# Kernel optimization log

Hardware: AMD Instinct MI355X
Metric: run time of the kernel (lower is better)

Reference implementation:

```python
import jax, jax.numpy as jnp
import numpy as np


def setup_inputs() -> dict:
    key = jax.random.key(0)
    ks = jax.random.split(key, 16)
    B, T, E, H, V = 64, 24, 512, 1024, 32000
    A = H  # attention_dim == hidden_size in original init
    s = 0.02  # init scale
    n = lambda k, shape: (jax.random.normal(k, shape, jnp.float32) * s)
    return {
        "features": jax.random.normal(ks[0], (B, E), jnp.float32),
        "captions": jax.random.randint(ks[1], (B, T), 0, V, dtype=jnp.int32),
        "lengths": jnp.full((B, 1), T + 1, dtype=jnp.int32),
        # learned parameters
        "emb": n(ks[2], (V, E)),
        "We": n(ks[3], (E, A)), "be": jnp.zeros((A,), jnp.float32),
        "Wd": n(ks[4], (H, A)), "bd": jnp.zeros((A,), jnp.float32),
        "va": n(ks[5], (A,)), "ba": jnp.zeros((), jnp.float32),
        "Wih": n(ks[6], (E, H)), "bih": jnp.zeros((H,), jnp.float32),
        "Wic": n(ks[7], (E, H)), "bic": jnp.zeros((H,), jnp.float32),
        "Wfb": n(ks[8], (H, E)), "bfb": jnp.zeros((E,), jnp.float32),
        "Wi": n(ks[9], (2 * E, 4 * H)), "Wh": n(ks[10], (H, 4 * H)),
        "bl": jnp.zeros((4 * H,), jnp.float32),
        "Wo": n(ks[11], (H, V)), "bo": jnp.zeros((V,), jnp.float32),
    }


def reference(features, captions, lengths, emb, We, be, Wd, bd, va, ba,
              Wih, bih, Wic, bic, Wfb, bfb, Wi, Wh, bl, Wo, bo):
    T = captions.shape[1]
    # embeddings = [features ; embed(captions)] -> [B, T+1, E]
    embeds = jnp.concatenate([features[:, None, :], emb[captions]], axis=1)
    mean_e = embeds.mean(axis=1)
    h = mean_e @ Wih + bih  # init_h
    c = mean_e @ Wic + bic  # init_c
    att1 = embeds @ We + be  # encoder projection, precomputed [B, L, A]

    def step(carry, emb_t):
        h, c = carry
        # additive attention over the full encoded sequence
        score = jnp.einsum('bla,a->bl', jax.nn.relu(att1 + (h @ Wd + bd)[:, None, :]), va) + ba
        alpha = jax.nn.softmax(score, axis=1)
        awe = jnp.einsum('bl,ble->be', alpha, embeds)
        gate = jax.nn.sigmoid(h @ Wfb + bfb)
        x = jnp.concatenate([emb_t, gate * awe], axis=-1)  # [B, 2E]
        z = x @ Wi + h @ Wh + bl
        i, f, g, o = jnp.split(z, 4, axis=-1)  # torch LSTM gate order i,f,g,o
        c = jax.nn.sigmoid(f) * c + jax.nn.sigmoid(i) * jnp.tanh(g)
        h = jax.nn.sigmoid(o) * jnp.tanh(c)
        return (h, c), h @ Wo + bo

    emb_seq = jnp.swapaxes(embeds[:, :T, :], 0, 1)  # [T, B, E]
    (_, _), logits = jax.lax.scan(step, (h, c), emb_seq)
    return jnp.swapaxes(logits, 0, 1)  # [B, T, V]
```

## Files before the change

### kernel.cpp

```cpp
#include <hip/hip_runtime.h>
#include <cstdio>
#include <cstdint>

#define B_ 64
#define T_ 24
#define L_ 25
#define E_ 512
#define H_ 1024
#define A_ 1024
#define V_ 32000
#define HCAT 5632

#define NKY_H 12
#define NKY_Z 6

typedef unsigned short u16;
typedef short bf16x8 __attribute__((ext_vector_type(8)));
typedef float f32x4 __attribute__((ext_vector_type(4)));

__device__ __forceinline__ u16 f2bf(float f) {
    union { float f; unsigned int u; } v; v.f = f;
    unsigned int u = v.u;
    unsigned int r = (u + 0x7FFFu + ((u >> 16) & 1u)) >> 16;
    return (u16)r;
}
__device__ __forceinline__ float bf2f(u16 h) {
    union { unsigned int u; float f; } v; v.u = ((unsigned int)h) << 16;
    return v.f;
}
__device__ __forceinline__ void splitbf(float a, u16& hi, u16& lo) {
    hi = f2bf(a);
    lo = f2bf(a - bf2f(hi));
}
__device__ __forceinline__ float sigf(float x) { return 1.f / (1.f + __expf(-x)); }

__device__ __forceinline__ void gload16(const u16* g, u16* l) {
    __builtin_amdgcn_global_load_lds(
        (const __attribute__((address_space(1))) unsigned int*)g,
        (__attribute__((address_space(3))) unsigned int*)l, 16, 0, 0);
}


__global__ void build_embeds(const float* __restrict__ features, const int* __restrict__ captions,
                             const float* __restrict__ emb, float* __restrict__ embeds,
                             float* __restrict__ mean_eT, u16* __restrict__ embsL2,
                             u16* __restrict__ embsA2) {
    int b = blockIdx.x; int e = threadIdx.x;
    float s = 0.f;
    for (int l = 0; l < L_; ++l) {
        float w;
        if (l == 0) w = features[b * E_ + e];
        else {
            int cap = captions[b * T_ + (l - 1)];
            w = emb[(size_t)cap * E_ + e];
        }
        embeds[(size_t)(b * L_ + l) * E_ + e] = w;
        s += w;
        u16 hi, lo; splitbf(w, hi, lo);
        size_t rl = (size_t)(b * L_ + l) * 1536;
        embsL2[rl + e] = hi; embsL2[rl + 512 + e] = lo; embsL2[rl + 1024 + e] = hi;
        if (l < T_) {
            size_t ra = (size_t)(l * 64 + b) * 1536;
            embsA2[ra + e] = hi; embsA2[ra + 512 + e] = lo; embsA2[ra + 1024 + e] = hi;
        }
    }
    mean_eT[e * B_ + b] = s * (1.f / 25.f);
}

__global__ __launch_bounds__(256) void prep_weights(
    const float* __restrict__ Wo, const float* __restrict__ Wd, const float* __restrict__ Wfb,
    const float* __restrict__ Wh, const float* __restrict__ Wi, const float* __restrict__ We,
    u16* __restrict__ WoT, u16* __restrict__ WcatT2, u16* __restrict__ WiT2a,
    u16* __restrict__ WiT2b, u16* __restrict__ WeT2) {
    __shared__ float tile[32][33];
    int id = blockIdx.x;
    int tid = threadIdx.x, tx = tid & 31, ty = tid >> 5;
    if (id < 32000) {
        int nx = id % 1000, ky = id / 1000;
        int n0 = nx * 32, k0 = ky * 32;
        for (int i = ty; i < 32; i += 8)
            tile[i][tx] = Wo[(size_t)(k0 + i) * V_ + n0 + tx];
        __syncthreads();
        for (int i = ty; i < 32; i += 8)
            WoT[(size_t)(n0 + i) * H_ + k0 + tx] = f2bf(tile[tx][i]);
        return;
    }
    id -= 32000;
    const float* W; u16* dst; int K, srcld, tilesx;
    if (id < 1024)      {             W = Wd;  dst = WcatT2;                        K = 1024; srcld = 1024; tilesx = 32; }
    else if (id < 1536) { id -= 1024; W = Wfb; dst = WcatT2 + (size_t)1024 * 3072;  K = 1024; srcld = 512;  tilesx = 16; }
    else if (id < 5632) { id -= 1536; W = Wh;  dst = WcatT2 + (size_t)1536 * 3072;  K = 1024; srcld = 4096; tilesx = 128; }
    else if (id < 7680) { id -= 5632; W = Wi;  dst = WiT2a;                         K = 512;  srcld = 4096; tilesx = 128; }
    else if (id < 9728) { id -= 7680; W = Wi + (size_t)512 * 4096; dst = WiT2b;     K = 512;  srcld = 4096; tilesx = 128; }
    else                { id -= 9728; W = We;  dst = WeT2;                          K = 512;  srcld = 1024; tilesx = 32; }
    int n0 = (id % tilesx) * 32, k0 = (id / tilesx) * 32;
    for (int i = ty; i < 32; i += 8)
        tile[i][tx] = W[(size_t)(k0 + i) * srcld + n0 + tx];
    __syncthreads();
    for (int i = ty; i < 32; i += 8) {
        float v = tile[tx][i];
        u16 hi, lo; splitbf(v, hi, lo);
        u16* d = dst + (size_t)(n0 + i) * (3 * K) + (k0 + tx);
        d[0] = hi; d[K] = hi; d[2 * K] = lo;
    }
}

__global__ __launch_bounds__(1024) void init_hc(const float* __restrict__ mean_eT,
                                                const float* __restrict__ Wih, const float* __restrict__ bih,
                                                const float* __restrict__ Wic, const float* __restrict__ bic,
                                                u16* __restrict__ h2, float* __restrict__ c) {
    int tid = threadIdx.x; int ny = tid & 15, r = tid >> 4;
    int col = blockIdx.x * 16 + ny;
    int cc = (col < H_) ? col : col - H_;
    const float* Wp = (col < H_) ? Wih : Wic;
    const float* bp = (col < H_) ? bih : bic;
    float acc = bp[cc];
    for (int k = 0; k < E_; ++k) acc += mean_eT[k * B_ + r] * Wp[(size_t)k * H_ + cc];
    if (col < H_) {
        u16 hi, lo; splitbf(acc, hi, lo);
        h2[(size_t)r * 3072 + cc] = hi;
        h2[(size_t)r * 3072 + 1024 + cc] = lo;
        h2[(size_t)r * 3072 + 2048 + cc] = hi;
    } else c[r * H_ + cc] = acc;
}

template<int BM, int BN>
__global__ __launch_bounds__(256) void gemm_split(const u16* __restrict__ A2, const u16* __restrict__ B2T,
                                                  const float* __restrict__ bias, float* __restrict__ C,
                                                  int K3, int ldc) {
    constexpr int LDS = 40;
    __shared__ u16 As[BM * LDS];
    __shared__ u16 Bs[BN * LDS];
    constexpr int FM = BM / 32, FN = BN / 32;
    constexpr int ACH = BM / 64, BCH = BN / 64;
    int m0 = blockIdx.x * BM, n0 = blockIdx.y * BN;
    int tid = threadIdx.x, lane = tid & 63, wid = tid >> 6;
    int wm = wid >> 1, wn = wid & 1;

    f32x4 acc[FM][FN];
#pragma unroll
    for (int m = 0; m < FM; ++m)
#pragma unroll
        for (int n = 0; n < FN; ++n) acc[m][n] = (f32x4){0.f, 0.f, 0.f, 0.f};

    const u16* agp[ACH]; u16* asw[ACH];
    const u16* bgp[BCH]; u16* bsw[BCH];
#pragma unroll
    for (int i = 0; i < ACH; ++i) {
        int id = i * 256 + tid; int row = id >> 2, q = id & 3;
        agp[i] = A2 + (size_t)(m0 + row) * K3 + q * 8;
        asw[i] = As + row * LDS + q * 8;
    }
#pragma unroll
    for (int i = 0; i < BCH; ++i) {
        int id = i * 256 + tid; int row = id >> 2, q = id & 3;
        bgp[i] = B2T + (size_t)(n0 + row) * K3 + q * 8;
        bsw[i] = Bs + row * LDS + q * 8;
    }
    int rsel = lane & 15, kg = (lane >> 4) * 8;
    const u16* ard[FM]; const u16* brd[FN];
#pragma unroll
    for (int m = 0; m < FM; ++m) ard[m] = As + (wm * (BM / 2) + m * 16 + rsel) * LDS + kg;
#pragma unroll
    for (int n = 0; n < FN; ++n) brd[n] = Bs + (wn * (BN / 2) + n * 16 + rsel) * LDS + kg;

    uint4 ar[ACH], br[BCH];
#pragma unroll
    for (int i = 0; i < ACH; ++i) ar[i] = *(const uint4*)(agp[i]);
#pragma unroll
    for (int i = 0; i < BCH; ++i) br[i] = *(const uint4*)(bgp[i]);

    int nk = K3 / 32;
    for (int k = 0; k < nk; ++k) {
#pragma unroll
        for (int i = 0; i < ACH; ++i) *(uint4*)(asw[i]) = ar[i];
#pragma unroll
        for (int i = 0; i < BCH; ++i) *(uint4*)(bsw[i]) = br[i];
        __syncthreads();
        if (k + 1 < nk) {
            int kt = (k + 1) * 32;
#pragma unroll
            for (int i = 0; i < ACH; ++i) ar[i] = *(const uint4*)(agp[i] + kt);
#pragma unroll
            for (int i = 0; i < BCH; ++i) br[i] = *(const uint4*)(bgp[i] + kt);
        }
        bf16x8 aF[FM], bF[FN];
#pragma unroll
        for (int m = 0; m < FM; ++m) aF[m] = *(const bf16x8*)(ard[m]);
#pragma unroll
        for (int n = 0; n < FN; ++n) bF[n] = *(const bf16x8*)(brd[n]);
#pragma unroll
        for (int m = 0; m < FM; ++m)
#pragma unroll
            for (int n = 0; n < FN; ++n)
                acc[m][n] = __builtin_amdgcn_mfma_f32_16x16x32_bf16(aF[m], bF[n], acc[m][n], 0, 0, 0);
        __syncthreads();
    }

    int r4 = (lane >> 4) * 4, cn = lane & 15;
#pragma unroll
    for (int n = 0; n < FN; ++n) {
        int gcol = n0 + wn * (BN / 2) + n * 16 + cn;
        float bv = bias[gcol];
#pragma unroll
        for (int m = 0; m < FM; ++m) {
            int gr = m0 + wm * (BM / 2) + m * 16 + r4;
#pragma unroll
            for (int reg = 0; reg < 4; ++reg)
                C[(size_t)(gr + reg) * ldc + gcol] = acc[m][n][reg] + bv;
        }
    }
}

template<int KITERS>
__global__ __launch_bounds__(256, 2) void gemm_sk(const u16* __restrict__ A2, const u16* __restrict__ B2T,
                                                  float* __restrict__ part, int K3, int N) {
    constexpr int BK = 128;
    constexpr int LDS = BK + 8;
    __shared__ u16 As[64 * LDS];
    __shared__ u16 Bs[64 * LDS];
    int n0 = blockIdx.x * 64;
    int ky = blockIdx.y;
    int k0 = ky * (BK * KITERS);
    int tid = threadIdx.x, lane = tid & 63, wid = tid >> 6;
    int wm = wid >> 1, wn = wid & 1;

    f32x4 acc[2][2];
#pragma unroll
    for (int m = 0; m < 2; ++m)
#pragma unroll
        for (int n = 0; n < 2; ++n) acc[m][n] = (f32x4){0.f, 0.f, 0.f, 0.f};

    int srow = tid >> 4, scq = tid & 15;
    const u16* agp[4]; u16* asw[4];
    const u16* bgp[4]; u16* bsw[4];
#pragma unroll
    for (int i = 0; i < 4; ++i) {
        int row = srow + i * 16;
        agp[i] = A2 + (size_t)row * K3 + k0 + scq * 8;
        asw[i] = As + row * LDS + scq * 8;
        bgp[i] = B2T + (size_t)(n0 + row) * K3 + k0 + scq * 8;
        bsw[i] = Bs + row * LDS + scq * 8;
    }
    int rsel = lane & 15, kg = (lane >> 4) * 8;
    const u16* ard[2]; const u16* brd[2];
#pragma unroll
    for (int m = 0; m < 2; ++m) ard[m] = As + (wm * 32 + m * 16 + rsel) * LDS + kg;
#pragma unroll
    for (int n = 0; n < 2; ++n) brd[n] = Bs + (wn * 32 + n * 16 + rsel) * LDS + kg;

    uint4 ar[4], br[4];
#pragma unroll
    for (int i = 0; i < 4; ++i) { ar[i] = *(const uint4*)(agp[i]); br[i] = *(const uint4*)(bgp[i]); }

    for (int it = 0; it < KITERS; ++it) {
#pragma unroll
        for (int i = 0; i < 4; ++i) { *(uint4*)(asw[i]) = ar[i]; *(uint4*)(bsw[i]) = br[i]; }
        __syncthreads();
        if (it + 1 < KITERS) {
            int kt = (it + 1) * BK;
#pragma unroll
            for (int i = 0; i < 4; ++i) {
                ar[i] = *(const uint4*)(agp[i] + kt);
                br[i] = *(const uint4*)(bgp[i] + kt);
            }
        }
#pragma unroll
        for (int kk = 0; kk < BK / 32; ++kk) {
            bf16x8 aF[2], bF[2];
#pragma unroll
            for (int m = 0; m < 2; ++m) aF[m] = *(const bf16x8*)(ard[m] + kk * 32);
#pragma unroll
            for (int n = 0; n < 2; ++n) bF[n] = *(const bf16x8*)(brd[n] + kk * 32);
#pragma unroll
            for (int m = 0; m < 2; ++m)
#pragma unroll
                for (int n = 0; n < 2; ++n)
                    acc[m][n] = __builtin_amdgcn_mfma_f32_16x16x32_bf16(aF[m], bF[n], acc[m][n], 0, 0, 0);
        }
        __syncthreads();
    }

    float* p = part + (size_t)ky * 64 * N;
    int r4 = (lane >> 4) * 4, cn = lane & 15;
#pragma unroll
    for (int n = 0; n < 2; ++n) {
        int gcol = n0 + wn * 32 + n * 16 + cn;
#pragma unroll
        for (int m = 0; m < 2; ++m) {
            int gr = wm * 32 + m * 16 + r4;
#pragma unroll
            for (int reg = 0; reg < 4; ++reg)
                p[(size_t)(gr + reg) * N + gcol] = acc[m][n][reg];
        }
    }
}


__global__ __launch_bounds__(256) void step_attn(const float* __restrict__ hpart, const float* __restrict__ att1,
                                                 const float* __restrict__ embeds, const float* __restrict__ va,
                                                 const float* __restrict__ bd, const float* __restrict__ bfb,
                                                 u16* __restrict__ x2s) {
    __shared__ float proj_s[1024], va_s[1024], sc_s[32], al_s[32];
    int b = blockIdx.x; int tid = threadIdx.x; int lane = tid & 63; int w = tid >> 6;
    for (int i = tid; i < 1024; i += 256) {
        float s = bd[i];
#pragma unroll
        for (int ky = 0; ky < NKY_H; ++ky) s += hpart[(size_t)ky * 64 * HCAT + b * HCAT + i];
        proj_s[i] = s; va_s[i] = va[i];
    }
    __syncthreads();
    for (int l = w; l < L_; l += 4) {
        const float* arow = att1 + (size_t)(b * L_ + l) * A_;
        float p = 0.f;
        for (int a = lane; a < A_; a += 64) {
            float v = arow[a] + proj_s[a];
            p += fmaxf(v, 0.f) * va_s[a];
        }
        for (int off = 32; off; off >>= 1) p += __shfl_down(p, off);
        if (lane == 0) sc_s[l] = p;
    }
    __syncthreads();
    if (w == 0) {
        float s = (lane < L_) ? sc_s[lane] : -1e30f;
        float m = s;
        for (int off = 32; off; off >>= 1) m = fmaxf(m, __shfl_xor(m, off));
        float e = (lane < L_) ? __expf(s - m) : 0.f;
        float sum = e;
        for (int off = 32; off; off >>= 1) sum += __shfl_xor(sum, off);
        if (lane < L_) al_s[lane] = e / sum;
    }
    __syncthreads();
    for (int e = tid; e < E_; e += 256) {
        float aw = 0.f;
        for (int l = 0; l < L_; ++l) aw += al_s[l] * embeds[(size_t)(b * L_ + l) * E_ + e];
        float gp = bfb[e];
#pragma unroll
        for (int ky = 0; ky < NKY_H; ++ky) gp += hpart[(size_t)ky * 64 * HCAT + b * HCAT + 1024 + e];
        float v = sigf(gp) * aw;
        u16 hi, lo; splitbf(v, hi, lo);
        x2s[(size_t)b * 1536 + e] = hi;
        x2s[(size_t)b * 1536 + 512 + e] = lo;
        x2s[(size_t)b * 1536 + 1024 + e] = hi;
    }
}

__global__ __launch_bounds__(256) void step_lstm(const float* __restrict__ zpart, const float* __restrict__ P1,
                                                 const float* __restrict__ hpart, float* __restrict__ c,
                                                 u16* __restrict__ h2, u16* __restrict__ hs_bf, int t) {
    int idx = blockIdx.x * 256 + threadIdx.x;
    int b = idx >> 10, n = idx & 1023;
    float zv[4];
#pragma unroll
    for (int g = 0; g < 4; ++g) {
        int col = g * 1024 + n;
        float s = P1[(size_t)(t * 64 + b) * 4096 + col];
#pragma unroll
        for (int ky = 0; ky < NKY_Z; ++ky) s += zpart[(size_t)ky * 64 * 4096 + b * 4096 + col];
#pragma unroll
        for (int ky = 0; ky < NKY_H; ++ky) s += hpart[(size_t)ky * 64 * HCAT + b * HCAT + 1536 + col];
        zv[g] = s;
    }
    float cold = c[b * H_ + n];
    float cnew = sigf(zv[1]) * cold + sigf(zv[0]) * tanhf(zv[2]);
    float hh = sigf(zv[3]) * tanhf(cnew);
    c[b * H_ + n] = cnew;
    u16 hi, lo; splitbf(hh, hi, lo);
    h2[(size_t)b * 3072 + n] = hi;
    h2[(size_t)b * 3072 + 1024 + n] = lo;
    h2[(size_t)b * 3072 + 2048 + n] = hi;
    hs_bf[(size_t)(t * 64 + b) * 1024 + n] = f2bf(hh);
}

#define BMG 128
#define BNG 128
#define NWG_M (T_ * B_ / BMG)
#define NWG_N (V_ / BNG)
#define NWG (NWG_M * NWG_N)

__global__ __launch_bounds__(256) void gemm_logits(const u16* __restrict__ Abf, const u16* __restrict__ Bbf,
                                                   const float* __restrict__ bo, float* __restrict__ out) {
    __shared__ u16 As[BMG * 32];
    __shared__ u16 Bs[BNG * 32];
    int lid = blockIdx.x;
    int wg = (lid & 7) * (NWG / 8) + (lid >> 3);
    int m0 = (wg % NWG_M) * BMG;
    int n0 = (wg / NWG_M) * BNG;
    int tid = threadIdx.x; int lane = tid & 63; int wid = tid >> 6;
    int wm = wid >> 1, wn = wid & 1;

    f32x4 acc[4][4];
#pragma unroll
    for (int m = 0; m < 4; ++m)
#pragma unroll
        for (int n = 0; n < 4; ++n) acc[m][n] = (f32x4){0.f, 0.f, 0.f, 0.f};

    int srow = wid * 32 + (lane >> 2);
    int sch = (lane & 3) * 8;
    const u16* agA0 = Abf + (size_t)(m0 + srow) * H_ + sch;
    const u16* agA1 = agA0 + (size_t)16 * H_;
    const u16* agB0 = Bbf + (size_t)(n0 + srow) * H_ + sch;
    const u16* agB1 = agB0 + (size_t)16 * H_;
    u16* lA0 = As + (wid * 32) * 32;
    u16* lA1 = As + (wid * 32 + 16) * 32;
    u16* lB0 = Bs + (wid * 32) * 32;
    u16* lB1 = Bs + (wid * 32 + 16) * 32;

    int rsel = (lane & 15);
    int kg = (lane >> 4) * 8;
    const u16* ard[4]; const u16* brd[4];
#pragma unroll
    for (int m = 0; m < 4; ++m) {
        ard[m] = As + (wm * 64 + m * 16 + rsel) * 32 + kg;
        brd[m] = Bs + (wn * 64 + m * 16 + rsel) * 32 + kg;
    }

    for (int kt = 0; kt < H_; kt += 32) {
        gload16(agA0 + kt, lA0);
        gload16(agA1 + kt, lA1);
        gload16(agB0 + kt, lB0);
        gload16(agB1 + kt, lB1);
        __syncthreads();
        bf16x8 aF[4], bF[4];
#pragma unroll
        for (int m = 0; m < 4; ++m) aF[m] = *(const bf16x8*)(ard[m]);
#pragma unroll
        for (int n = 0; n < 4; ++n) bF[n] = *(const bf16x8*)(brd[n]);
#pragma unroll
        for (int m = 0; m < 4; ++m)
#pragma unroll
            for (int n = 0; n < 4; ++n)
                acc[m][n] = __builtin_amdgcn_mfma_f32_16x16x32_bf16(aF[m], bF[n], acc[m][n], 0, 0, 0);
        __syncthreads();
    }

    int r4 = (lane >> 4) * 4;
    int cn = lane & 15;
#pragma unroll
    for (int n = 0; n < 4; ++n) {
        int gn = n0 + wn * 64 + n * 16 + cn;
        float bv = bo[gn];
#pragma unroll
        for (int m = 0; m < 4; ++m) {
            int gmb = m0 + wm * 64 + m * 16 + r4;
#pragma unroll
            for (int reg = 0; reg < 4; ++reg) {
                int gm = gmb + reg;
                int b = gm & 63, t = gm >> 6;
                out[(size_t)(b * T_ + t) * V_ + gn] = acc[m][n][reg] + bv;
            }
        }
    }
}

extern "C" void kernel_launch(void* const* d_in, const int* in_sizes, int n_in,
                              void* d_out, int out_size, void* d_ws, size_t ws_size,
                              hipStream_t stream) {
    const float* features = (const float*)d_in[0];
    const int*   captions = (const int*)d_in[1];
    const float* emb = (const float*)d_in[3];
    const float* We  = (const float*)d_in[4];
    const float* be  = (const float*)d_in[5];
    const float* Wd  = (const float*)d_in[6];
    const float* bd  = (const float*)d_in[7];
    const float* va  = (const float*)d_in[8];
    const float* Wih = (const float*)d_in[10];
    const float* bih = (const float*)d_in[11];
    const float* Wic = (const float*)d_in[12];
    const float* bic = (const float*)d_in[13];
    const float* Wfb = (const float*)d_in[14];
    const float* bfb = (const float*)d_in[15];
    const float* Wi  = (const float*)d_in[16];
    const float* Wh  = (const float*)d_in[17];
    const float* bl  = (const float*)d_in[18];
    const float* Wo  = (const float*)d_in[19];
    const float* bo  = (const float*)d_in[20];
    float* out = (float*)d_out;

    char* ws = (char*)d_ws; size_t wo = 0;
    auto walloc = [&](size_t bytes) -> void* {
        void* p = ws + wo; wo += (bytes + 255) & ~(size_t)255; return p;
    };
    float* embeds  = (float*)walloc((size_t)B_ * L_ * E_ * 4);
    float* mean_eT = (float*)walloc((size_t)E_ * B_ * 4);
    u16*   embsL2  = (u16*)walloc((size_t)B_ * L_ * 1536 * 2);
    u16*   embsA2  = (u16*)walloc((size_t)T_ * B_ * 1536 * 2);
    u16*   h2      = (u16*)walloc((size_t)B_ * 3072 * 2);
    float* c       = (float*)walloc((size_t)B_ * H_ * 4);
    u16*   x2s     = (u16*)walloc((size_t)B_ * 1536 * 2);
    u16*   hs_bf   = (u16*)walloc((size_t)T_ * B_ * H_ * 2);
    u16*   WoT     = (u16*)walloc((size_t)V_ * H_ * 2);
    float* hpart   = (float*)walloc((size_t)NKY_H * B_ * HCAT * 4);
    float* zpart   = (float*)walloc((size_t)NKY_Z * B_ * 4096 * 4);
    if (wo > ws_size) {
        fprintf(stderr, "kernel_launch: ws too small: need %zu have %zu\n", wo, ws_size);
        return;
    }

    char* ob = (char*)d_out; size_t oo = 0;
    auto oalloc = [&](size_t bytes) -> void* {
        void* p = ob + oo; oo += (bytes + 255) & ~(size_t)255; return p;
    };
    float* P1     = (float*)oalloc((size_t)T_ * B_ * 4096 * 4);
    u16*   WcatT2 = (u16*)oalloc((size_t)HCAT * 3072 * 2);
    u16*   WiT2a  = (u16*)oalloc((size_t)4096 * 1536 * 2);
    u16*   WiT2b  = (u16*)oalloc((size_t)4096 * 1536 * 2);
    u16*   WeT2   = (u16*)oalloc((size_t)1024 * 1536 * 2);
    float* att1   = (float*)oalloc((size_t)B_ * L_ * A_ * 4);

    build_embeds<<<B_, E_, 0, stream>>>(features, captions, emb, embeds, mean_eT, embsL2, embsA2);
    prep_weights<<<32000 + 10240, 256, 0, stream>>>(Wo, Wd, Wfb, Wh, Wi, We,
                                                    WoT, WcatT2, WiT2a, WiT2b, WeT2);
    init_hc<<<2 * H_ / 16, 1024, 0, stream>>>(mean_eT, Wih, bih, Wic, bic, h2, c);
    gemm_split<64, 64><<<dim3(1600 / 64, 1024 / 64), 256, 0, stream>>>(embsL2, WeT2, be, att1, 1536, 1024);
    gemm_split<128, 64><<<dim3(1536 / 128, 4096 / 64), 256, 0, stream>>>(embsA2, WiT2a, bl, P1, 1536, 4096);

    for (int t = 0; t < T_; ++t) {
        gemm_sk<2><<<dim3(HCAT / 64, NKY_H), 256, 0, stream>>>(h2, WcatT2, hpart, 3072, HCAT);
        step_attn<<<B_, 256, 0, stream>>>(hpart, att1, embeds, va, bd, bfb, x2s);
        gemm_sk<2><<<dim3(4096 / 64, NKY_Z), 256, 0, stream>>>(x2s, WiT2b, zpart, 1536, 4096);
        step_lstm<<<B_ * H_ / 256, 256, 0, stream>>>(zpart, P1, hpart, c, h2, hs_bf, t);
    }

    gemm_logits<<<NWG, 256, 0, stream>>>(hs_bf, WoT, bo, out);
}
```

Before: 2.435 ms.

## Double K tile in logits GEMM and XOR-swizzle shared memory layout

The logits GEMM now stages a K slice of 64 per iteration instead of 32. This halves the number of barrier pairs and makes each global-to-LDS load round larger. The shared-memory rows are XOR-swizzled by row index so the wider 128-byte rows avoid LDS bank conflicts on the MFMA fragment reads. LDS use per block doubles, which may lower occupancy, and correctness depends on the swizzle matching between the direct-to-LDS loads and the reads.

```diff
diff --git a/kernel.cpp b/kernel.cpp
--- a/kernel.cpp
+++ b/kernel.cpp
@@ -374,14 +374,15 @@
 
 #define BMG 128
 #define BNG 128
+#define BKG 64
 #define NWG_M (T_ * B_ / BMG)
 #define NWG_N (V_ / BNG)
 #define NWG (NWG_M * NWG_N)
 
 __global__ __launch_bounds__(256) void gemm_logits(const u16* __restrict__ Abf, const u16* __restrict__ Bbf,
                                                    const float* __restrict__ bo, float* __restrict__ out) {
-    __shared__ u16 As[BMG * 32];
-    __shared__ u16 Bs[BNG * 32];
+    __shared__ u16 As[BMG * BKG];
+    __shared__ u16 Bs[BNG * BKG];
     int lid = blockIdx.x;
     int wg = (lid & 7) * (NWG / 8) + (lid >> 3);
     int m0 = (wg % NWG_M) * BMG;
@@ -395,37 +396,53 @@
 #pragma unroll
         for (int n = 0; n < 4; ++n) acc[m][n] = (f32x4){0.f, 0.f, 0.f, 0.f};
 
-    int srow = wid * 32 + (lane >> 2);
-    int sch = (lane & 3) * 8;
-    const u16* agA0 = Abf + (size_t)(m0 + srow) * H_ + sch;
-    const u16* agA1 = agA0 + (size_t)16 * H_;
-    const u16* agB0 = Bbf + (size_t)(n0 + srow) * H_ + sch;
-    const u16* agB1 = agB0 + (size_t)16 * H_;
-    u16* lA0 = As + (wid * 32) * 32;
-    u16* lA1 = As + (wid * 32 + 16) * 32;
-    u16* lB0 = Bs + (wid * 32) * 32;
-    u16* lB1 = Bs + (wid * 32 + 16) * 32;
-
-    int rsel = (lane & 15);
-    int kg = (lane >> 4) * 8;
-    const u16* ard[4]; const u16* brd[4];
+    int rowoff = lane >> 3;
+    int gch = (lane & 7) ^ (rowoff & 7);
+    const u16* agA[4]; const u16* agB[4];
+    u16* lA[4]; u16* lB[4];
+#pragma unroll
+    for (int i = 0; i < 4; ++i) {
+        int r = wid * 32 + i * 8 + rowoff;
+        agA[i] = Abf + (size_t)(m0 + r) * H_ + gch * 8;
+        agB[i] = Bbf + (size_t)(n0 + r) * H_ + gch * 8;
+        lA[i] = As + (wid * 32 + i * 8) * BKG;
+        lB[i] = Bs + (wid * 32 + i * 8) * BKG;
+    }
+
+    int rsel = lane & 15;
+    int q0 = lane >> 4;
+    int rs7 = rsel & 7;
+    const u16 *ard0[4], *ard1[4], *brd0[4], *brd1[4];
 #pragma unroll
     for (int m = 0; m < 4; ++m) {
-        ard[m] = As + (wm * 64 + m * 16 + rsel) * 32 + kg;
-        brd[m] = Bs + (wn * 64 + m * 16 + rsel) * 32 + kg;
-    }
-
-    for (int kt = 0; kt < H_; kt += 32) {
-        gload16(agA0 + kt, lA0);
-        gload16(agA1 + kt, lA1);
-        gload16(agB0 + kt, lB0);
-        gload16(agB1 + kt, lB1);
+        int arow = wm * 64 + m * 16 + rsel;
+        int brow = wn * 64 + m * 16 + rsel;
+        ard0[m] = As + arow * BKG + (q0 ^ rs7) * 8;
+        ard1[m] = As + arow * BKG + ((q0 + 4) ^ rs7) * 8;
+        brd0[m] = Bs + brow * BKG + (q0 ^ rs7) * 8;
+        brd1[m] = Bs + brow * BKG + ((q0 + 4) ^ rs7) * 8;
+    }
+
+    for (int kt = 0; kt < H_; kt += BKG) {
+#pragma unroll
+        for (int i = 0; i < 4; ++i) gload16(agA[i] + kt, lA[i]);
+#pragma unroll
+        for (int i = 0; i < 4; ++i) gload16(agB[i] + kt, lB[i]);
         __syncthreads();
         bf16x8 aF[4], bF[4];
 #pragma unroll
-        for (int m = 0; m < 4; ++m) aF[m] = *(const bf16x8*)(ard[m]);
-#pragma unroll
-        for (int n = 0; n < 4; ++n) bF[n] = *(const bf16x8*)(brd[n]);
+        for (int m = 0; m < 4; ++m) aF[m] = *(const bf16x8*)(ard0[m]);
+#pragma unroll
+        for (int n = 0; n < 4; ++n) bF[n] = *(const bf16x8*)(brd0[n]);
+#pragma unroll
+        for (int m = 0; m < 4; ++m)
+#pragma unroll
+            for (int n = 0; n < 4; ++n)
+                acc[m][n] = __builtin_amdgcn_mfma_f32_16x16x32_bf16(aF[m], bF[n], acc[m][n], 0, 0, 0);
+#pragma unroll
+        for (int m = 0; m < 4; ++m) aF[m] = *(const bf16x8*)(ard1[m]);
+#pragma unroll
+        for (int n = 0; n < 4; ++n) bF[n] = *(const bf16x8*)(brd1[n]);
 #pragma unroll
         for (int m = 0; m < 4; ++m)
 #pragma unroll
```

After: 2.440 ms. About the same (+0.2%).
